# Performance work log

Measured on AMD Instinct MI355X. Metric: run time of the kernel, lower is better.

Reference implementation:

```python
import jax, jax.numpy as jnp
import numpy as np

WS = 8        # world_size (tp group size)
M = 8192      # global M, divisible by WS
N = 4096
LOCAL_K = 1024  # K // WS


def setup_inputs() -> dict:
    key = jax.random.key(0)
    k1, k2 = jax.random.split(key)
    # Per-rank K-sharded activation and weight (transpose_weight=False => weight is [N, local_K])
    inp = jax.random.normal(k1, (WS, M, LOCAL_K), dtype=jnp.float32)
    wgt = jax.random.normal(k2, (WS, N, LOCAL_K), dtype=jnp.float32) * 0.02
    return {"input": inp, "weight": wgt}


def reference(input, weight):
    """GEMM + reduce-scatter across the TP group.

    Each rank r computes partial_r = input[r] @ weight[r].T  -> [M, N].
    Reduce: full = sum_r partial_r. Scatter: rank r receives rows
    [r*M/WS : (r+1)*M/WS]. We return the scattered result for all ranks
    stacked on the leading axis: [WS, M//WS, N].
    """
    # Contract over both the rank axis (the reduce) and local_K in one einsum.
    full = jnp.einsum('rmk,rnk->mn', input, weight)  # [M, N]
    return full.reshape(WS, M // WS, N)
```

## Files before the change

### kernel.cpp

```cpp
#include <hip/hip_runtime.h>
#include <hip/hip_bf16.h>


#define M_TOT 8192
#define N_TOT 4096
#define LK    1024
#define NR    8
#define K_TOT (NR * LK)
#define NT    (K_TOT / 64)

typedef float f32x4 __attribute__((ext_vector_type(4)));
typedef short s16x8 __attribute__((ext_vector_type(8)));
typedef const __attribute__((address_space(1))) unsigned int* gptr_t;
typedef __attribute__((address_space(3))) unsigned int* lptr_t;

__device__ inline short f2bf(float f) {
    __hip_bfloat16 h = __float2bfloat16(f);
    return *reinterpret_cast<short*>(&h);
}

__global__ __launch_bounds__(256)
void cvt_bf16(const float* __restrict__ in, short* __restrict__ out,
              int row_shift, int row_mask) {
    const int row = blockIdx.x * 2 + (threadIdx.x >> 7);
    const int c   = (threadIdx.x & 127) * 8;
    const int r   = row >> row_shift;
    const int m   = row & row_mask;
    const float* src = in + ((size_t)row << 10) + c;
    f32x4 v0 = *(const f32x4*)src;
    f32x4 v1 = *(const f32x4*)(src + 4);
    s16x8 o;
    #pragma unroll
    for (int j = 0; j < 4; ++j) { o[j] = f2bf(v0[j]); o[j + 4] = f2bf(v1[j]); }
    *(s16x8*)(out + ((size_t)m << 13) + ((size_t)r << 10) + c) = o;
}


__device__ __forceinline__ void stage_half(const short* srcBase, short* ldsOp,
                                           int half, int ktile, int wid) {
    #pragma unroll
    for (int q = 0; q < 2; ++q) {
        const short* src = srcBase + (size_t)(half * 128 + q * 8) * K_TOT + ktile * 64;
        short* dst = ldsOp + (half * 128 + wid * 16 + q * 8) * 64;
        __builtin_amdgcn_global_load_lds((gptr_t)src, (lptr_t)dst, 16, 0, 0);
    }
}

template<int C>
__device__ __forceinline__ void read_a_pair(s16x8 (&afr)[8][2], const short* lAc,
                                            int wm, int r15, int kg) {
    #pragma unroll
    for (int fo = 0; fo < 2; ++fo)
        #pragma unroll
        for (int ks = 0; ks < 2; ++ks) {
            const int row = C * 64 + wm * 32 + fo * 16 + r15;
            const int off = row * 64 + ((((ks << 2) | kg) ^ (row & 7)) << 3);
            afr[C * 2 + fo][ks] = *(const s16x8*)(lAc + off);
        }
}

__device__ __forceinline__ void read_b(s16x8 (&bfr)[4][2], const short* lBc,
                                       int wn, int r15, int kg) {
    #pragma unroll
    for (int n = 0; n < 4; ++n)
        #pragma unroll
        for (int ks = 0; ks < 2; ++ks) {
            const int row = wn * 64 + n * 16 + r15;
            const int off = row * 64 + ((((ks << 2) | kg) ^ (row & 7)) << 3);
            bfr[n][ks] = *(const s16x8*)(lBc + off);
        }
}

template<int N>
__device__ __forceinline__ void read_b_one(s16x8 (&bfr)[4][2], const short* lBc,
                                           int wn, int r15, int kg) {
    #pragma unroll
    for (int ks = 0; ks < 2; ++ks) {
        const int row = wn * 64 + N * 16 + r15;
        const int off = row * 64 + ((((ks << 2) | kg) ^ (row & 7)) << 3);
        bfr[N][ks] = *(const s16x8*)(lBc + off);
    }
}

template<int Q>
__device__ __forceinline__ void mfma_quad(f32x4 (&acc)[8][4], s16x8 (&afr)[8][2],
                                          s16x8 (&bfr)[4][2]) {
    __builtin_amdgcn_s_setprio(1);
    #pragma unroll
    for (int fo = 0; fo < 2; ++fo)
        #pragma unroll
        for (int n = 0; n < 4; ++n)
            #pragma unroll
            for (int ks = 0; ks < 2; ++ks)
                acc[Q * 2 + fo][n] = __builtin_amdgcn_mfma_f32_16x16x32_bf16(
                    afr[Q * 2 + fo][ks], bfr[n][ks], acc[Q * 2 + fo][n], 0, 0, 0);
    __builtin_amdgcn_s_setprio(0);
}

template<int N>
__device__ __forceinline__ void mfma_n3(f32x4 (&acc)[8][4], s16x8 (&afr)[8][2],
                                        s16x8 (&bfr)[4][2]) {
    #pragma unroll
    for (int fo = 0; fo < 2; ++fo)
        #pragma unroll
        for (int ks = 0; ks < 2; ++ks)
            acc[6 + fo][N] = __builtin_amdgcn_mfma_f32_16x16x32_bf16(
                afr[6 + fo][ks], bfr[N][ks], acc[6 + fo][N], 0, 0, 0);
}

#define MEMCLOB asm volatile("" ::: "memory")
#define BAR     __builtin_amdgcn_s_barrier()
#define SCHED0  __builtin_amdgcn_sched_barrier(0)

#define TILE_BODY(P) do {                                                     \
    const int t = 2 * t2 + (P);                                               \
    const short* lAc = smem + ((P) << 15);                                    \
    short* bufN = smem + (((P) ^ 1) << 15);                                   \
    short* bufC = smem + ((P) << 15);                                         \
       \
    read_a_pair<1>(afr, lAc, wm, r15, kg);                                    \
    if (t + 1 < NT) stage_half(srcA, bufN, 1, t + 1, wid);                    \
    MEMCLOB; BAR;                                                             \
    asm volatile("s_waitcnt lgkmcnt(4)" ::: "memory"); SCHED0;                \
    mfma_quad<0>(acc, afr, bfr);                                              \
    MEMCLOB; BAR;                                                             \
      \
    read_a_pair<2>(afr, lAc, wm, r15, kg);                                    \
    if (t + 2 < NT) stage_half(srcB, bufC + 16384, 0, t + 2, wid);            \
    MEMCLOB; BAR;                                                             \
    asm volatile("s_waitcnt lgkmcnt(4)" ::: "memory"); SCHED0;                \
    mfma_quad<1>(acc, afr, bfr);                                              \
    MEMCLOB; BAR;                                                             \
                                             \
    read_a_pair<3>(afr, lAc, wm, r15, kg);                                    \
    if (t + 2 < NT) stage_half(srcB, bufC + 16384, 1, t + 2, wid);            \
    MEMCLOB; BAR;                                                             \
    asm volatile("s_waitcnt lgkmcnt(4)" ::: "memory"); SCHED0;                \
    mfma_quad<2>(acc, afr, bfr);                                              \
    MEMCLOB; BAR;                                                             \
    \
    \
    \
    \
    \
    if (t < NT - 2)       asm volatile("s_waitcnt vmcnt(4)" ::: "memory");    \
    else if (t == NT - 2) asm volatile("s_waitcnt vmcnt(0)" ::: "memory");    \
    MEMCLOB; BAR;                                                             \
    if (t + 2 < NT) stage_half(srcA, bufC, 0, t + 2, wid);                    \
    if (t + 1 < NT) {                                                         \
        read_a_pair<0>(afr, bufN, wm, r15, kg);                               \
        asm volatile("s_waitcnt lgkmcnt(4)" ::: "memory"); SCHED0;            \
        __builtin_amdgcn_s_setprio(1);                                        \
        mfma_n3<0>(acc, afr, bfr);                                            \
        read_b_one<0>(bfr, bufN + 16384, wn, r15, kg);                        \
        mfma_n3<1>(acc, afr, bfr);                                            \
        read_b_one<1>(bfr, bufN + 16384, wn, r15, kg);                        \
        mfma_n3<2>(acc, afr, bfr);                                            \
        read_b_one<2>(bfr, bufN + 16384, wn, r15, kg);                        \
        mfma_n3<3>(acc, afr, bfr);                                            \
        read_b_one<3>(bfr, bufN + 16384, wn, r15, kg);                        \
        __builtin_amdgcn_s_setprio(0);                                        \
    } else {                                                                  \
        asm volatile("s_waitcnt lgkmcnt(0)" ::: "memory"); SCHED0;            \
        __builtin_amdgcn_s_setprio(1);                                        \
        mfma_n3<0>(acc, afr, bfr);                                            \
        mfma_n3<1>(acc, afr, bfr);                                            \
        mfma_n3<2>(acc, afr, bfr);                                            \
        mfma_n3<3>(acc, afr, bfr);                                            \
        __builtin_amdgcn_s_setprio(0);                                        \
    }                                                                         \
    MEMCLOB; BAR;                                                             \
} while (0)

__global__ __launch_bounds__(512, 2)
void gemm8(const short* __restrict__ A, const short* __restrict__ B,
           float* __restrict__ C) {
    extern __shared__ short smem[];

    const int tid  = threadIdx.x;
    const int lane = tid & 63;
    const int wid  = tid >> 6;
    const int wm   = wid >> 2;
    const int wn   = wid & 3;
    const int r15  = lane & 15;
    const int kg   = lane >> 4;
    const int l8   = lane >> 3;
    const int g16  = (lane & 7) ^ l8;

    const int bid = blockIdx.x;
    const int sw  = (bid & 7) * 64 + (bid >> 3);
    const int bm  = sw >> 4;
    const int bn  = sw & 15;

    const short* srcA = A + (size_t)(bm * 256 + wid * 16 + l8) * K_TOT + g16 * 8;
    const short* srcB = B + (size_t)(bn * 256 + wid * 16 + l8) * K_TOT + g16 * 8;

    stage_half(srcB, smem + 16384, 0, 0, wid);
    stage_half(srcB, smem + 16384, 1, 0, wid);
    stage_half(srcA, smem,         0, 0, wid);
    stage_half(srcA, smem,         1, 0, wid);
    stage_half(srcB, smem + 49152, 0, 1, wid);
    stage_half(srcB, smem + 49152, 1, 1, wid);
    stage_half(srcA, smem + 32768, 0, 1, wid);
    asm volatile("s_waitcnt vmcnt(6)" ::: "memory");
    MEMCLOB; BAR;

    f32x4 acc[8][4];
    #pragma unroll
    for (int f = 0; f < 8; ++f)
        #pragma unroll
        for (int n = 0; n < 4; ++n)
            acc[f][n] = (f32x4){0.f, 0.f, 0.f, 0.f};

    s16x8 afr[8][2];
    s16x8 bfr[4][2];

    read_b(bfr, smem + 16384, wn, r15, kg);
    read_a_pair<0>(afr, smem, wm, r15, kg);

    for (int t2 = 0; t2 < NT / 2; ++t2) {
        TILE_BODY(0);
        TILE_BODY(1);
    }

    float* Cp = C + (size_t)(bm * 256 + wm * 32 + kg * 4) * N_TOT
                  + bn * 256 + wn * 64 + r15;
    #pragma unroll
    for (int f = 0; f < 8; ++f)
        #pragma unroll
        for (int n = 0; n < 4; ++n)
            #pragma unroll
            for (int jj = 0; jj < 4; ++jj) {
                const int roff = (f >> 1) * 64 + (f & 1) * 16 + jj;
                Cp[(size_t)roff * N_TOT + n * 16] = acc[f][n][jj];
            }
}

#define PAD_ROW 40
__global__ __launch_bounds__(256, 2)
void gemm_rs_fused(const float* __restrict__ A, const float* __restrict__ B,
                   float* __restrict__ C) {
    __shared__ short lA[128 * PAD_ROW];
    __shared__ short lB[128 * PAD_ROW];
    const int bid = blockIdx.x;
    const int sw  = (bid & 7) * (int)(gridDim.x >> 3) + (bid >> 3);
    const int bm = sw >> 5, bn = sw & 31;
    const int tid = threadIdx.x, lane = tid & 63, wid = tid >> 6;
    const int wr = wid >> 1, wc = wid & 1, r15 = lane & 15, kg = lane >> 4;
    const int srow = tid >> 1, scg = tid & 1;
    const float* gA = A + ((size_t)(bm * 128 + srow) << 10) + scg * 16;
    const float* gB = B + ((size_t)(bn * 128 + srow) << 10) + scg * 16;
    short* wpA = lA + srow * PAD_ROW + scg * 16;
    short* wpB = lB + srow * PAD_ROW + scg * 16;
    const short* rpA = lA + (wr * 64 + r15) * PAD_ROW + kg * 8;
    const short* rpB = lB + (wc * 64 + r15) * PAD_ROW + kg * 8;
    f32x4 acc[4][4];
    #pragma unroll
    for (int i = 0; i < 4; ++i)
        #pragma unroll
        for (int j = 0; j < 4; ++j) acc[i][j] = (f32x4){0.f, 0.f, 0.f, 0.f};
    for (int t = 0; t < K_TOT / 32; ++t) {
        const int r = t >> 5, k0 = (t & 31) << 5;
        const float* pA = gA + (size_t)r * (M_TOT * LK) + k0;
        const float* pB = gB + (size_t)r * (N_TOT * LK) + k0;
        f32x4 va[4], vb[4];
        #pragma unroll
        for (int q = 0; q < 4; ++q) va[q] = *(const f32x4*)(pA + q * 4);
        #pragma unroll
        for (int q = 0; q < 4; ++q) vb[q] = *(const f32x4*)(pB + q * 4);
        __syncthreads();
        s16x8 oa0, oa1, ob0, ob1;
        #pragma unroll
        for (int q = 0; q < 2; ++q)
            #pragma unroll
            for (int i = 0; i < 4; ++i) {
                oa0[q * 4 + i] = f2bf(va[q][i]);
                oa1[q * 4 + i] = f2bf(va[q + 2][i]);
                ob0[q * 4 + i] = f2bf(vb[q][i]);
                ob1[q * 4 + i] = f2bf(vb[q + 2][i]);
            }
        *(s16x8*)(wpA) = oa0; *(s16x8*)(wpA + 8) = oa1;
        *(s16x8*)(wpB) = ob0; *(s16x8*)(wpB + 8) = ob1;
        __syncthreads();
        s16x8 af[4], bfr2[4];
        #pragma unroll
        for (int i = 0; i < 4; ++i) af[i]   = *(const s16x8*)(rpA + i * 16 * PAD_ROW);
        #pragma unroll
        for (int i = 0; i < 4; ++i) bfr2[i] = *(const s16x8*)(rpB + i * 16 * PAD_ROW);
        #pragma unroll
        for (int i = 0; i < 4; ++i)
            #pragma unroll
            for (int j = 0; j < 4; ++j)
                acc[i][j] = __builtin_amdgcn_mfma_f32_16x16x32_bf16(
                    af[i], bfr2[j], acc[i][j], 0, 0, 0);
    }
    float* Cp = C + (size_t)(bm * 128 + wr * 64 + kg * 4) * N_TOT
                  + bn * 128 + wc * 64 + r15;
    #pragma unroll
    for (int i = 0; i < 4; ++i)
        #pragma unroll
        for (int j = 0; j < 4; ++j)
            #pragma unroll
            for (int jj = 0; jj < 4; ++jj)
                Cp[(size_t)(i * 16 + jj) * N_TOT + j * 16] = acc[i][j][jj];
}

extern "C" void kernel_launch(void* const* d_in, const int* in_sizes, int n_in,
                              void* d_out, int out_size, void* d_ws, size_t ws_size,
                              hipStream_t stream) {
    const float* A = (const float*)d_in[0];
    const float* B = (const float*)d_in[1];
    float* C = (float*)d_out;

    const size_t needA = (size_t)M_TOT * K_TOT * 2;
    const size_t needB = (size_t)N_TOT * K_TOT * 2;

    if (ws_size >= needA + needB) {
        short* Abf = (short*)d_ws;
        short* Bbf = (short*)((char*)d_ws + needA);
        cvt_bf16<<<dim3(NR * M_TOT / 2), dim3(256), 0, stream>>>(A, Abf, 13, 8191);
        cvt_bf16<<<dim3(NR * N_TOT / 2), dim3(256), 0, stream>>>(B, Bbf, 12, 4095);
        gemm8<<<dim3((M_TOT / 256) * (N_TOT / 256)), dim3(512), 131072, stream>>>(Abf, Bbf, C);
    } else {
        gemm_rs_fused<<<dim3((M_TOT / 128) * (N_TOT / 128)), dim3(256), 0, stream>>>(A, B, C);
    }
}
```

Measured before the change: 517.0 us.

## Use 4-wave blocks with 128-column warp tiles in bf16 GEMM

Shrinks the GEMM workgroup from 8 waves to 4 waves. Each wave now covers 128 output columns instead of 64, with a 8x8 accumulator array, and the A fragments are double-buffered in a 2-slot array. Staging issues 4 loads per thread per half-tile, and the vmcnt waits change to match. The aim is to raise per-wave register reuse of A fragments and reduce LDS read traffic per MFMA. The cost is much higher register pressure (256 accumulator floats per lane) and fewer waves to hide latency.

```diff
diff --git a/kernel.cpp b/kernel.cpp
--- a/kernel.cpp
+++ b/kernel.cpp
@@ -39,15 +39,15 @@
 __device__ __forceinline__ void stage_half(const short* srcBase, short* ldsOp,
                                            int half, int ktile, int wid) {
     #pragma unroll
-    for (int q = 0; q < 2; ++q) {
-        const short* src = srcBase + (size_t)(half * 128 + q * 8) * K_TOT + ktile * 64;
-        short* dst = ldsOp + (half * 128 + wid * 16 + q * 8) * 64;
+    for (int q = 0; q < 4; ++q) {
+        const short* src = srcBase + (size_t)(half * 128 + q * 32) * K_TOT + ktile * 64;
+        short* dst = ldsOp + (half * 128 + q * 32 + wid * 8) * 64;
         __builtin_amdgcn_global_load_lds((gptr_t)src, (lptr_t)dst, 16, 0, 0);
     }
 }
 
 template<int C>
-__device__ __forceinline__ void read_a_pair(s16x8 (&afr)[8][2], const short* lAc,
+__device__ __forceinline__ void read_a_pair(s16x8 (&afr)[2][2][2], const short* lAc,
                                             int wm, int r15, int kg) {
     #pragma unroll
     for (int fo = 0; fo < 2; ++fo)
@@ -55,76 +55,80 @@
         for (int ks = 0; ks < 2; ++ks) {
             const int row = C * 64 + wm * 32 + fo * 16 + r15;
             const int off = row * 64 + ((((ks << 2) | kg) ^ (row & 7)) << 3);
-            afr[C * 2 + fo][ks] = *(const s16x8*)(lAc + off);
+            afr[C & 1][fo][ks] = *(const s16x8*)(lAc + off);
         }
 }
 
-__device__ __forceinline__ void read_b(s16x8 (&bfr)[4][2], const short* lBc,
-                                       int wn, int r15, int kg) {
-    #pragma unroll
-    for (int n = 0; n < 4; ++n)
+__device__ __forceinline__ void read_b_all(s16x8 (&bfr)[8][2], const short* lBc,
+                                           int wn, int r15, int kg) {
+    #pragma unroll
+    for (int n = 0; n < 8; ++n)
         #pragma unroll
         for (int ks = 0; ks < 2; ++ks) {
-            const int row = wn * 64 + n * 16 + r15;
+            const int row = wn * 128 + n * 16 + r15;
             const int off = row * 64 + ((((ks << 2) | kg) ^ (row & 7)) << 3);
             bfr[n][ks] = *(const s16x8*)(lBc + off);
         }
 }
 
 template<int N>
-__device__ __forceinline__ void read_b_one(s16x8 (&bfr)[4][2], const short* lBc,
+__device__ __forceinline__ void read_b_one(s16x8 (&bfr)[8][2], const short* lBc,
                                            int wn, int r15, int kg) {
     #pragma unroll
     for (int ks = 0; ks < 2; ++ks) {
-        const int row = wn * 64 + N * 16 + r15;
+        const int row = wn * 128 + N * 16 + r15;
         const int off = row * 64 + ((((ks << 2) | kg) ^ (row & 7)) << 3);
         bfr[N][ks] = *(const s16x8*)(lBc + off);
     }
 }
 
 template<int Q>
-__device__ __forceinline__ void mfma_quad(f32x4 (&acc)[8][4], s16x8 (&afr)[8][2],
-                                          s16x8 (&bfr)[4][2]) {
+__device__ __forceinline__ void mfma_quad(f32x4 (&acc)[8][8], s16x8 (&afr)[2][2][2],
+                                          s16x8 (&bfr)[8][2]) {
     __builtin_amdgcn_s_setprio(1);
     #pragma unroll
     for (int fo = 0; fo < 2; ++fo)
         #pragma unroll
-        for (int n = 0; n < 4; ++n)
+        for (int n = 0; n < 8; ++n)
             #pragma unroll
             for (int ks = 0; ks < 2; ++ks)
                 acc[Q * 2 + fo][n] = __builtin_amdgcn_mfma_f32_16x16x32_bf16(
-                    afr[Q * 2 + fo][ks], bfr[n][ks], acc[Q * 2 + fo][n], 0, 0, 0);
+                    afr[Q & 1][fo][ks], bfr[n][ks], acc[Q * 2 + fo][n], 0, 0, 0);
     __builtin_amdgcn_s_setprio(0);
 }
 
 template<int N>
-__device__ __forceinline__ void mfma_n3(f32x4 (&acc)[8][4], s16x8 (&afr)[8][2],
-                                        s16x8 (&bfr)[4][2]) {
+__device__ __forceinline__ void mfma_n3(f32x4 (&acc)[8][8], s16x8 (&afr)[2][2][2],
+                                        s16x8 (&bfr)[8][2]) {
     #pragma unroll
     for (int fo = 0; fo < 2; ++fo)
         #pragma unroll
         for (int ks = 0; ks < 2; ++ks)
             acc[6 + fo][N] = __builtin_amdgcn_mfma_f32_16x16x32_bf16(
-                afr[6 + fo][ks], bfr[N][ks], acc[6 + fo][N], 0, 0, 0);
+                afr[1][fo][ks], bfr[N][ks], acc[6 + fo][N], 0, 0, 0);
 }
 
 #define MEMCLOB asm volatile("" ::: "memory")
 #define BAR     __builtin_amdgcn_s_barrier()
 #define SCHED0  __builtin_amdgcn_sched_barrier(0)
+
+#define INTERLEAVE_STEP(N) do {                                               \
+    mfma_n3<N>(acc, afr, bfr);                                                \
+    read_b_one<N>(bfr, bufN + 16384, wn, r15, kg); } while (0)
 
 #define TILE_BODY(P) do {                                                     \
     const int t = 2 * t2 + (P);                                               \
     const short* lAc = smem + ((P) << 15);                                    \
     short* bufN = smem + (((P) ^ 1) << 15);                                   \
     short* bufC = smem + ((P) << 15);                                         \
-       \
+        \
     read_a_pair<1>(afr, lAc, wm, r15, kg);                                    \
     if (t + 1 < NT) stage_half(srcA, bufN, 1, t + 1, wid);                    \
     MEMCLOB; BAR;                                                             \
     asm volatile("s_waitcnt lgkmcnt(4)" ::: "memory"); SCHED0;                \
     mfma_quad<0>(acc, afr, bfr);                                              \
     MEMCLOB; BAR;                                                             \
-      \
+                                             \
     read_a_pair<2>(afr, lAc, wm, r15, kg);                                    \
     if (t + 2 < NT) stage_half(srcB, bufC + 16384, 0, t + 2, wid);            \
     MEMCLOB; BAR;                                                             \
@@ -141,9 +145,7 @@
     \
     \
     \
-    \
-    \
-    if (t < NT - 2)       asm volatile("s_waitcnt vmcnt(4)" ::: "memory");    \
+    if (t < NT - 2)       asm volatile("s_waitcnt vmcnt(8)" ::: "memory");    \
     else if (t == NT - 2) asm volatile("s_waitcnt vmcnt(0)" ::: "memory");    \
     MEMCLOB; BAR;                                                             \
     if (t + 2 < NT) stage_half(srcA, bufC, 0, t + 2, wid);                    \
@@ -151,37 +153,33 @@
         read_a_pair<0>(afr, bufN, wm, r15, kg);                               \
         asm volatile("s_waitcnt lgkmcnt(4)" ::: "memory"); SCHED0;            \
         __builtin_amdgcn_s_setprio(1);                                        \
-        mfma_n3<0>(acc, afr, bfr);                                            \
-        read_b_one<0>(bfr, bufN + 16384, wn, r15, kg);                        \
-        mfma_n3<1>(acc, afr, bfr);                                            \
-        read_b_one<1>(bfr, bufN + 16384, wn, r15, kg);                        \
-        mfma_n3<2>(acc, afr, bfr);                                            \
-        read_b_one<2>(bfr, bufN + 16384, wn, r15, kg);                        \
-        mfma_n3<3>(acc, afr, bfr);                                            \
-        read_b_one<3>(bfr, bufN + 16384, wn, r15, kg);                        \
+        INTERLEAVE_STEP(0); INTERLEAVE_STEP(1);                               \
+        INTERLEAVE_STEP(2); INTERLEAVE_STEP(3);                               \
+        INTERLEAVE_STEP(4); INTERLEAVE_STEP(5);                               \
+        INTERLEAVE_STEP(6); INTERLEAVE_STEP(7);                               \
         __builtin_amdgcn_s_setprio(0);                                        \
     } else {                                                                  \
         asm volatile("s_waitcnt lgkmcnt(0)" ::: "memory"); SCHED0;            \
         __builtin_amdgcn_s_setprio(1);                                        \
-        mfma_n3<0>(acc, afr, bfr);                                            \
-        mfma_n3<1>(acc, afr, bfr);                                            \
-        mfma_n3<2>(acc, afr, bfr);                                            \
-        mfma_n3<3>(acc, afr, bfr);                                            \
+        mfma_n3<0>(acc, afr, bfr); mfma_n3<1>(acc, afr, bfr);                 \
+        mfma_n3<2>(acc, afr, bfr); mfma_n3<3>(acc, afr, bfr);                 \
+        mfma_n3<4>(acc, afr, bfr); mfma_n3<5>(acc, afr, bfr);                 \
+        mfma_n3<6>(acc, afr, bfr); mfma_n3<7>(acc, afr, bfr);                 \
         __builtin_amdgcn_s_setprio(0);                                        \
     }                                                                         \
     MEMCLOB; BAR;                                                             \
 } while (0)
 
-__global__ __launch_bounds__(512, 2)
-void gemm8(const short* __restrict__ A, const short* __restrict__ B,
+__global__ __launch_bounds__(256, 1)
+void gemm4(const short* __restrict__ A, const short* __restrict__ B,
            float* __restrict__ C) {
     extern __shared__ short smem[];
 
     const int tid  = threadIdx.x;
     const int lane = tid & 63;
     const int wid  = tid >> 6;
-    const int wm   = wid >> 2;
-    const int wn   = wid & 3;
+    const int wm   = wid >> 1;
+    const int wn   = wid & 1;
     const int r15  = lane & 15;
     const int kg   = lane >> 4;
     const int l8   = lane >> 3;
@@ -192,8 +190,8 @@
     const int bm  = sw >> 4;
     const int bn  = sw & 15;
 
-    const short* srcA = A + (size_t)(bm * 256 + wid * 16 + l8) * K_TOT + g16 * 8;
-    const short* srcB = B + (size_t)(bn * 256 + wid * 16 + l8) * K_TOT + g16 * 8;
+    const short* srcA = A + (size_t)(bm * 256 + wid * 8 + l8) * K_TOT + g16 * 8;
+    const short* srcB = B + (size_t)(bn * 256 + wid * 8 + l8) * K_TOT + g16 * 8;
 
     stage_half(srcB, smem + 16384, 0, 0, wid);
     stage_half(srcB, smem + 16384, 1, 0, wid);
@@ -202,20 +200,20 @@
     stage_half(srcB, smem + 49152, 0, 1, wid);
     stage_half(srcB, smem + 49152, 1, 1, wid);
     stage_half(srcA, smem + 32768, 0, 1, wid);
-    asm volatile("s_waitcnt vmcnt(6)" ::: "memory");
+    asm volatile("s_waitcnt vmcnt(12)" ::: "memory");
     MEMCLOB; BAR;
 
-    f32x4 acc[8][4];
+    f32x4 acc[8][8];
     #pragma unroll
     for (int f = 0; f < 8; ++f)
         #pragma unroll
-        for (int n = 0; n < 4; ++n)
+        for (int n = 0; n < 8; ++n)
             acc[f][n] = (f32x4){0.f, 0.f, 0.f, 0.f};
 
-    s16x8 afr[8][2];
-    s16x8 bfr[4][2];
-
-    read_b(bfr, smem + 16384, wn, r15, kg);
+    s16x8 afr[2][2][2];
+    s16x8 bfr[8][2];
+
+    read_b_all(bfr, smem + 16384, wn, r15, kg);
     read_a_pair<0>(afr, smem, wm, r15, kg);
 
     for (int t2 = 0; t2 < NT / 2; ++t2) {
@@ -224,11 +222,11 @@
     }
 
     float* Cp = C + (size_t)(bm * 256 + wm * 32 + kg * 4) * N_TOT
-                  + bn * 256 + wn * 64 + r15;
+                  + bn * 256 + wn * 128 + r15;
     #pragma unroll
     for (int f = 0; f < 8; ++f)
         #pragma unroll
-        for (int n = 0; n < 4; ++n)
+        for (int n = 0; n < 8; ++n)
             #pragma unroll
             for (int jj = 0; jj < 4; ++jj) {
                 const int roff = (f >> 1) * 64 + (f & 1) * 16 + jj;
@@ -320,7 +318,7 @@
         short* Bbf = (short*)((char*)d_ws + needA);
         cvt_bf16<<<dim3(NR * M_TOT / 2), dim3(256), 0, stream>>>(A, Abf, 13, 8191);
         cvt_bf16<<<dim3(NR * N_TOT / 2), dim3(256), 0, stream>>>(B, Bbf, 12, 4095);
-        gemm8<<<dim3((M_TOT / 256) * (N_TOT / 256)), dim3(512), 131072, stream>>>(Abf, Bbf, C);
+        gemm4<<<dim3((M_TOT / 256) * (N_TOT / 256)), dim3(256), 131072, stream>>>(Abf, Bbf, C);
     } else {
         gemm_rs_fused<<<dim3((M_TOT / 128) * (N_TOT / 128)), dim3(256), 0, stream>>>(A, B, C);
     }
```

New measurement: 518.7 us. Within noise of the previous version (+0.3%).
